# Optimization experiments

Measured on AMD Instinct MI355X. Metric: run time of the kernel, lower is better.

The kernel has to match this reference:

```python
import jax, jax.numpy as jnp
import numpy as np

B, S, D, H, DK, FF, NQ = 4, 1024, 512, 64, 8, 2048, 8


def _layernorm(x, w, b, eps=1e-5):
    m = x.mean(-1, keepdims=True)
    v = ((x - m) ** 2).mean(-1, keepdims=True)
    return (x - m) / jnp.sqrt(v + eps) * w + b


def setup_inputs() -> dict:
    key = jax.random.key(0)
    ks = jax.random.split(key, 24)
    std = 0.02
    inp = {
        "x": jax.random.normal(ks[0], (B, S, D), dtype=jnp.float32),
        "Wq": jax.random.normal(ks[1], (D, D)) * std,
        "bq": jnp.zeros((D,)),
        "Wk": jax.random.normal(ks[2], (D, D)) * std,
        "bk": jnp.zeros((D,)),
        "Wv": jax.random.normal(ks[3], (D, D)) * std,
        "bv": jnp.zeros((D,)),
        "theta_attn": jax.random.normal(ks[4], (DK,)) * 0.1,  # trainable RX angles
        "gate_attn": jnp.asarray(1.0, dtype=jnp.float32),
        "Wo": jax.random.normal(ks[5], (D, D)) * std,
        "bo": jnp.zeros((D,)),
        "ln1_w": jnp.ones((D,)),
        "ln1_b": jnp.zeros((D,)),
        "W1": jax.random.normal(ks[6], (FF, NQ)) * std,
        "b1": jnp.zeros((FF,)),
        "W2": jax.random.normal(ks[7], (D, FF)) * std,
        "b2": jnp.zeros((D,)),
        "phi_ffn": jax.random.normal(ks[8], (NQ,)) * 0.1,  # trainable RY angles
        "gate_ffn": jnp.asarray(1.0, dtype=jnp.float32),
        "ln2_w": jnp.ones((D,)),
        "ln2_b": jnp.zeros((D,)),
    }
    return inp


def _attention(x, Wq, bq, Wk, bk, Wv, bv, theta, gate, Wo, bo):
    q = x @ Wq.T + bq
    k = x @ Wk.T + bk
    v = x @ Wv.T + bv
    sep = lambda t: t.reshape(B, S, H, DK).transpose(0, 2, 1, 3)  # [B,H,S,DK]
    qh, kh, vh = sep(q), sep(k), sep(v)
    scores = jnp.einsum("bhsd,bhtd->bhst", qh, kh) / np.sqrt(DK)
    probs = jax.nn.softmax(scores, axis=-1)
    classical = jnp.einsum("bhst,bhtd->bhsd", probs, vh)
    classical = classical.transpose(0, 2, 1, 3).reshape(B, S, D)
    # Quantum head: RX(x_i) then RX(theta_i) -> RX(x_i+theta_i), CNOT ring, <Z_j>.
    # Analytic expectations: <Z_0> = prod_{k=1..DK-1} cos(a_k);
    #                        <Z_j> = prod_{k=0..j}    cos(a_k)   (j >= 1).
    cos_a = jnp.cos(qh + theta)  # [B,H,S,DK]
    cp = jnp.cumprod(cos_a, axis=-1)
    z0 = jnp.prod(cos_a[..., 1:], axis=-1, keepdims=True)
    quantum = jnp.concatenate([z0, cp[..., 1:]], axis=-1)  # [B,H,S,DK]
    quantum = quantum.transpose(0, 2, 1, 3).reshape(B, S, D)
    out = gate * quantum + (1.0 - gate) * classical
    return out @ Wo.T + bo


def _ffn(x, W1, b1, W2, b2, phi, gate):
    xs = x[..., :NQ]  # encoder uses first NQ features
    # Quantum: RX(x_i) then RY(phi_i), measure <Z_i> = cos(x_i)*cos(phi_i).
    qm = jnp.cos(xs) * jnp.cos(phi)
    quantum = jax.nn.relu(qm @ W1.T + b1) @ W2.T + b2
    classical = jax.nn.relu(xs @ W1.T + b1) @ W2.T + b2
    return gate * quantum + (1.0 - gate) * classical


def reference(x, Wq, bq, Wk, bk, Wv, bv, theta_attn, gate_attn, Wo, bo,
              ln1_w, ln1_b, W1, b1, W2, b2, phi_ffn, gate_ffn, ln2_w, ln2_b):
    attn_out = _attention(x, Wq, bq, Wk, bk, Wv, bv, theta_attn, gate_attn, Wo, bo)
    x1 = _layernorm(x + attn_out, ln1_w, ln1_b)
    ffn_out = _ffn(x1, W1, b1, W2, b2, phi_ffn, gate_ffn)
    return _layernorm(x1 + ffn_out, ln2_w, ln2_b)
```

## Files before the change

kernel.cpp:

```cpp
#include <hip/hip_runtime.h>
#include <hip/hip_bf16.h>


typedef short short8 __attribute__((ext_vector_type(8)));
typedef float floatx4 __attribute__((ext_vector_type(4)));

__device__ __forceinline__ unsigned short f2bf_bits(float f) {
  __hip_bfloat16 h = __float2bfloat16(f);
  return *reinterpret_cast<unsigned short*>(&h);
}
__device__ __forceinline__ float bfbits2f(unsigned short u) {
  union { unsigned int u; float f; } c;
  c.u = (unsigned int)u << 16;
  return c.f;
}

#define GLOBAL_LOAD_LDS16(g, l)                                               \
  __builtin_amdgcn_global_load_lds(                                           \
      (const __attribute__((address_space(1))) void*)(g),                     \
      (__attribute__((address_space(3))) void*)(l), 16, 0, 0)

#define WAIT_VMCNT0()   asm volatile("s_waitcnt vmcnt(0)" ::: "memory")
#define WAIT_VMCNT8()   asm volatile("s_waitcnt vmcnt(8)" ::: "memory")
#define WAIT_VMCNT10()  asm volatile("s_waitcnt vmcnt(10)" ::: "memory")
#define WAIT_VMCNT16()  asm volatile("s_waitcnt vmcnt(16)" ::: "memory")
#define WAIT_LGKM0()    asm volatile("s_waitcnt lgkmcnt(0)" ::: "memory")
#define BARRIER()       __builtin_amdgcn_s_barrier()
#define CFENCE()        asm volatile("" ::: "memory")

__device__ __forceinline__ void gemm_core_ks(
    const __hip_bfloat16* __restrict__ A,
    const __hip_bfloat16* __restrict__ W,
    int K, int kbeg, int ntiles, long m0, long n0, int lane,
    __hip_bfloat16* sh, floatx4 acc[4][4])
{
  const int srow = lane >> 3;
  const int gchunk = (lane & 7) ^ srow;
  const int frow = lane & 15;
  const int fk = lane >> 4;

  auto stage = [&](int kt, __hip_bfloat16* buf) {
#pragma unroll
    for (int ib = 0; ib < 8; ++ib) {
      const int row = ib * 8 + srow;
      GLOBAL_LOAD_LDS16(A + (m0 + row) * K + kt + gchunk * 8, buf + ib * 512);
      GLOBAL_LOAD_LDS16(W + (n0 + row) * K + kt + gchunk * 8, buf + 4096 + ib * 512);
    }
  };

  WAIT_LGKM0();
  stage(kbeg, sh);
  if (ntiles > 1) stage(kbeg + 64, sh + 8192);

  for (int t = 0; t < ntiles; ++t) {
    __hip_bfloat16* buf = sh + (t & 1) * 8192;
    if (t < ntiles - 1) { WAIT_VMCNT16(); }
    else               { WAIT_VMCNT0(); }

    short8 af[2][4], bf[2][4];
#pragma unroll
    for (int ks = 0; ks < 2; ++ks)
#pragma unroll
      for (int i = 0; i < 4; ++i) {
        const int ar = i * 16 + frow;
        af[ks][i] = *(const short8*)(buf + ar * 64 + (((ks * 4 + fk) ^ (ar & 7)) << 3));
        bf[ks][i] = *(const short8*)(buf + 4096 + ar * 64 + (((ks * 4 + fk) ^ (ar & 7)) << 3));
      }
    WAIT_LGKM0();
    if (t + 2 < ntiles) stage(kbeg + ((t + 2) << 6), buf);
#pragma unroll
    for (int ks = 0; ks < 2; ++ks)
#pragma unroll
      for (int i = 0; i < 4; ++i)
#pragma unroll
        for (int j = 0; j < 4; ++j)
          acc[i][j] = __builtin_amdgcn_mfma_f32_16x16x32_bf16(
              af[ks][i], bf[ks][j], acc[i][j], 0, 0, 0);
  }
}

__device__ __forceinline__ bool ks_reduce(
    floatx4 acc[4][4], __hip_bfloat16* sh, int wid, int lane)
{
  float* red = (float*)(sh + 16384);
  if (wid == 1) {
#pragma unroll
    for (int i = 0; i < 4; ++i)
#pragma unroll
      for (int j = 0; j < 4; ++j)
        *(floatx4*)(red + ((i * 4 + j) * 64 + lane) * 4) = acc[i][j];
    WAIT_LGKM0();
  }
  CFENCE(); BARRIER(); CFENCE();
  if (wid == 1) return false;
#pragma unroll
  for (int i = 0; i < 4; ++i)
#pragma unroll
    for (int j = 0; j < 4; ++j)
      acc[i][j] += *(const floatx4*)(red + ((i * 4 + j) * 64 + lane) * 4);
  return true;
}

__device__ __forceinline__ void store_f32(
    floatx4 acc[4][4], float* __restrict__ C, const float* __restrict__ bias,
    long m0, long n0, int lane)
{
  const int col_l = lane & 15;
  const int row_l = (lane >> 4) << 2;
#pragma unroll
  for (int j = 0; j < 4; ++j) {
    const long col = n0 + j * 16 + col_l;
    const float bv = bias[col];
#pragma unroll
    for (int i = 0; i < 4; ++i)
#pragma unroll
      for (int r = 0; r < 4; ++r)
        C[(m0 + i * 16 + row_l + r) * 512 + col] = acc[i][j][r] + bv;
  }
}

__device__ __forceinline__ void store_bf16(
    floatx4 acc[4][4], __hip_bfloat16* __restrict__ C,
    const float* __restrict__ bias, long m0, long n0, int lane)
{
  const int col_l = lane & 15;
  const int row_l = (lane >> 4) << 2;
#pragma unroll
  for (int j = 0; j < 4; ++j) {
    const long col = n0 + j * 16 + col_l;
    const float bv = bias[col];
#pragma unroll
    for (int i = 0; i < 4; ++i)
#pragma unroll
      for (int r = 0; r < 4; ++r)
        C[(m0 + i * 16 + row_l + r) * 512 + col] =
            __float2bfloat16(acc[i][j][r] + bv);
  }
}

__global__ __launch_bounds__(128) void gemm_qkv(
    const __hip_bfloat16* __restrict__ x_bf,
    const __hip_bfloat16* __restrict__ Wq,
    const __hip_bfloat16* __restrict__ Wk,
    const __hip_bfloat16* __restrict__ Wv,
    const float* __restrict__ bq, const float* __restrict__ bk,
    const float* __restrict__ bvv,
    __hip_bfloat16* __restrict__ mix,
    float* __restrict__ Qb, float* __restrict__ Kb, float* __restrict__ Vb,
    const float* __restrict__ theta, const float* __restrict__ gateA)
{
  const int z = blockIdx.z;
  const float g = *gateA;
  if (z > 0 && g == 1.0f) return;
  const __hip_bfloat16* W = (z == 0) ? Wq : (z == 1) ? Wk : Wv;
  const float* bias = (z == 0) ? bq : (z == 1) ? bk : bvv;
  float* Cf = (z == 0) ? Qb : (z == 1) ? Kb : Vb;

  __shared__ __align__(16) __hip_bfloat16 sh[32768];
  const int tid = threadIdx.x;
  const int wid = tid >> 6;
  const int lane = tid & 63;
  const long m0 = (long)blockIdx.x * 64;
  const long n0 = (long)blockIdx.y * 64;
  floatx4 acc[4][4];
#pragma unroll
  for (int i = 0; i < 4; ++i)
#pragma unroll
    for (int j = 0; j < 4; ++j) acc[i][j] = (floatx4){0.f, 0.f, 0.f, 0.f};

  gemm_core_ks(x_bf, W, 512, wid * 256, 4, m0, n0, lane, sh + wid * 16384, acc);
  if (!ks_reduce(acc, sh, wid, lane)) return;

  const int col_l = lane & 15;
  const int row_l = (lane >> 4) << 2;

  if (z > 0 || g != 1.0f) store_f32(acc, Cf, bias, m0, n0, lane);
  if (z == 0) {
    float* shf = (float*)sh;
    WAIT_LGKM0();
#pragma unroll
    for (int j = 0; j < 4; ++j) {
      const long col = n0 + j * 16 + col_l;
      const float bv = bias[col];
#pragma unroll
      for (int i = 0; i < 4; ++i)
#pragma unroll
        for (int r = 0; r < 4; ++r)
          shf[(i * 16 + row_l + r) * 64 + j * 16 + col_l] = acc[i][j][r] + bv;
    }
    WAIT_LGKM0();
    float th[8];
#pragma unroll
    for (int i = 0; i < 8; ++i) th[i] = theta[i];
#pragma unroll
    for (int t = 0; t < 8; ++t) {
      const int gidx = t * 64 + lane;
      const int row = gidx >> 3;
      const int hh = gidx & 7;
      const float* src = shf + row * 64 + hh * 8;
      float c[8];
#pragma unroll
      for (int i = 0; i < 8; ++i) c[i] = __cosf(src[i] + th[i]);
      float o[8];
      float p = c[1];
#pragma unroll
      for (int i = 2; i < 8; ++i) p *= c[i];
      o[0] = p;
      float cp = c[0];
#pragma unroll
      for (int i = 1; i < 8; ++i) { cp *= c[i]; o[i] = cp; }
      union { unsigned short u16[8]; uint4 v; } pk;
#pragma unroll
      for (int i = 0; i < 8; ++i) pk.u16[i] = f2bf_bits(o[i]);
      *(uint4*)(mix + (m0 + row) * 512 + n0 + hh * 8) = pk.v;
    }
  }
}

__global__ __launch_bounds__(512) void wo_lnffn(
    const __hip_bfloat16* __restrict__ A,
    const __hip_bfloat16* __restrict__ W,
    const float* __restrict__ bo,
    const float* __restrict__ x,
    const float* __restrict__ lw, const float* __restrict__ lb,
    float* __restrict__ x1, const float* __restrict__ phi,
    const float* __restrict__ W1,
    const float* __restrict__ b1,
    __hip_bfloat16* __restrict__ hq, __hip_bfloat16* __restrict__ hc,
    const float* __restrict__ gateF,
    __hip_bfloat16* __restrict__ mix_rw,
    const float* __restrict__ Qb, const float* __restrict__ Kb,
    const float* __restrict__ Vb, const float* __restrict__ gateA)
{
  __shared__ __align__(16) __hip_bfloat16 sh[68608];
  const int tid = threadIdx.x;
  const int wid = tid >> 6;
  const int lane = tid & 63;
  const long m0 = (long)blockIdx.x * 16;
  const long n0w = (long)wid * 64;

  const float g = *gateA;
  if (g != 1.0f) {
#pragma unroll 1
    for (int p = tid * 2; p < tid * 2 + 2; ++p) {
      const int r = p >> 6;
      const int h = p & 63;
      const long row = m0 + r;
      const int b = (int)(row >> 10);
      const long qoff = row * 512 + h * 8;
      float q[8];
#pragma unroll
      for (int i = 0; i < 8; ++i) q[i] = Qb[qoff + i] * 0.35355339059327373f;
      float m = -INFINITY, l = 0.0f, acc8[8];
#pragma unroll
      for (int i = 0; i < 8; ++i) acc8[i] = 0.0f;
      for (int t = 0; t < 1024; ++t) {
        const long koff = ((long)(b * 1024 + t)) * 512 + h * 8;
        const float* kr = Kb + koff;
        const float* vr = Vb + koff;
        float sc = 0.0f;
#pragma unroll
        for (int i = 0; i < 8; ++i) sc += q[i] * kr[i];
        float nm = fmaxf(m, sc);
        float corr = __expf(m - nm);
        float pp = __expf(sc - nm);
        l = l * corr + pp;
#pragma unroll
        for (int i = 0; i < 8; ++i) acc8[i] = acc8[i] * corr + pp * vr[i];
        m = nm;
      }
      const float inv = 1.0f / l;
      union { unsigned short u16[8]; uint4 v; } pk;
      pk.v = *(const uint4*)(mix_rw + qoff);
#pragma unroll
      for (int i = 0; i < 8; ++i) {
        float quant = bfbits2f(pk.u16[i]);
        pk.u16[i] = f2bf_bits(g * quant + (1.0f - g) * acc8[i] * inv);
      }
      *(uint4*)(mix_rw + qoff) = pk.v;
    }
    WAIT_VMCNT0();
    CFENCE(); BARRIER(); CFENCE();
  }

  const int srow = lane >> 3;
  const int gchunk = (lane & 7) ^ srow;
  const int frow = lane & 15;
  const int fk = lane >> 4;

  __hip_bfloat16* shA = sh;
  __hip_bfloat16* shW = sh + 3072 + wid * 8192;

  auto stageA = [&](int kt, int slot) {
    __hip_bfloat16* buf = shA + slot * 1024;
#pragma unroll
    for (int i = 0; i < 2; ++i) {
      const int row = i * 8 + srow;
      GLOBAL_LOAD_LDS16(A + (m0 + row) * 512 + kt + gchunk * 8, buf + i * 512);
    }
  };
  auto stageW = [&](int kt, int slot) {
    __hip_bfloat16* buf = shW + slot * 4096;
#pragma unroll
    for (int i = 0; i < 8; ++i) {
      const int row = i * 8 + srow;
      GLOBAL_LOAD_LDS16(W + (n0w + row) * 512 + kt + gchunk * 8, buf + i * 512);
    }
  };

  floatx4 acc[4];
#pragma unroll
  for (int j = 0; j < 4; ++j) acc[j] = (floatx4){0.f, 0.f, 0.f, 0.f};

  if (wid == 0) stageA(0, 0);
  stageW(0, 0);
  if (wid == 0) stageA(64, 1);
  stageW(64, 1);

  for (int t = 0; t < 8; ++t) {
    const int wslot = t & 1;
    const int aslot = t % 3;
    if (t < 7) { if (wid == 0) WAIT_VMCNT10(); else WAIT_VMCNT8(); }
    else       { WAIT_VMCNT0(); }
    BARRIER();

    short8 af[2], bf[2][4];
#pragma unroll
    for (int ks = 0; ks < 2; ++ks) {
      af[ks] = *(const short8*)(shA + aslot * 1024 + frow * 64 +
                                (((ks * 4 + fk) ^ (frow & 7)) << 3));
#pragma unroll
      for (int j = 0; j < 4; ++j) {
        const int wr = j * 16 + frow;
        bf[ks][j] = *(const short8*)(shW + wslot * 4096 + wr * 64 +
                                     (((ks * 4 + fk) ^ (wr & 7)) << 3));
      }
    }
    WAIT_LGKM0();
    if (t < 6) {
      if (wid == 0) stageA((t + 2) << 6, (t + 2) % 3);
      stageW((t + 2) << 6, wslot);
    }
#pragma unroll
    for (int ks = 0; ks < 2; ++ks)
#pragma unroll
      for (int j = 0; j < 4; ++j)
        acc[j] = __builtin_amdgcn_mfma_f32_16x16x32_bf16(
            af[ks], bf[ks][j], acc[j], 0, 0, 0);
  }

  BARRIER();

  float* attnL = (float*)sh;
  float* qmL = attnL + 16 * 516;
  float* xsL = qmL + 128;
  {
    const int col_l = lane & 15;
    const int row_l = (lane >> 4) << 2;
#pragma unroll
    for (int j = 0; j < 4; ++j) {
      const int c = (int)n0w + j * 16 + col_l;
      const float bv = bo[c];
#pragma unroll
      for (int r = 0; r < 4; ++r)
        attnL[(row_l + r) * 516 + c] = acc[j][r] + bv;
    }
  }
  WAIT_LGKM0();
  BARRIER();

  const int rr = tid >> 5;
  const int cl = tid & 31;
  const long rowg = m0 + rr;
  float sv[16];
  float sum = 0.f, ssq = 0.f;
#pragma unroll
  for (int i = 0; i < 16; ++i) {
    const int c = cl + i * 32;
    const float v = x[rowg * 512 + c] + attnL[rr * 516 + c];
    sv[i] = v; sum += v; ssq += v * v;
  }
#pragma unroll
  for (int off = 16; off > 0; off >>= 1) {
    sum += __shfl_xor(sum, off, 32);
    ssq += __shfl_xor(ssq, off, 32);
  }
  const float mean = sum * (1.0f / 512.0f);
  const float var = ssq * (1.0f / 512.0f) - mean * mean;
  const float rstd = rsqrtf(fmaxf(var, 0.0f) + 1e-5f);
#pragma unroll
  for (int i = 0; i < 16; ++i) {
    const int c = cl + i * 32;
    const float o = (sv[i] - mean) * rstd * lw[c] + lb[c];
    x1[rowg * 512 + c] = o;
    if (i == 0 && cl < 8) {
      qmL[rr * 8 + cl] = __cosf(o) * __cosf(phi[cl]);
      xsL[rr * 8 + cl] = o;
    }
  }
  WAIT_LGKM0();
  BARRIER();

  const int n4 = tid << 2;
  float w1r[4][8];
#pragma unroll
  for (int jr = 0; jr < 4; ++jr) {
    float4 wa = *(const float4*)(W1 + (long)(n4 + jr) * 8);
    float4 wb = *(const float4*)(W1 + (long)(n4 + jr) * 8 + 4);
    w1r[jr][0] = wa.x; w1r[jr][1] = wa.y; w1r[jr][2] = wa.z; w1r[jr][3] = wa.w;
    w1r[jr][4] = wb.x; w1r[jr][5] = wb.y; w1r[jr][6] = wb.z; w1r[jr][7] = wb.w;
  }
  float4 bb = *(const float4*)(b1 + n4);
  const float b1a[4] = {bb.x, bb.y, bb.z, bb.w};
  const float gv = *gateF;
#pragma unroll 2
  for (int r = 0; r < 16; ++r) {
    float qm8[8];
#pragma unroll
    for (int k = 0; k < 8; ++k) qm8[k] = qmL[r * 8 + k];
    union { unsigned short u16[4]; ushort4 v; } pk;
#pragma unroll
    for (int jr = 0; jr < 4; ++jr) {
      float a = b1a[jr];
#pragma unroll
      for (int k = 0; k < 8; ++k) a += qm8[k] * w1r[jr][k];
      pk.u16[jr] = f2bf_bits(fmaxf(a, 0.0f));
    }
    *(ushort4*)(hq + (m0 + r) * 2048 + n4) = pk.v;
    if (gv != 1.0f) {
      float xs8[8];
#pragma unroll
      for (int k = 0; k < 8; ++k) xs8[k] = xsL[r * 8 + k];
#pragma unroll
      for (int jr = 0; jr < 4; ++jr) {
        float a = b1a[jr];
#pragma unroll
        for (int k = 0; k < 8; ++k) a += xs8[k] * w1r[jr][k];
        pk.u16[jr] = f2bf_bits(fmaxf(a, 0.0f));
      }
      *(ushort4*)(hc + (m0 + r) * 2048 + n4) = pk.v;
    }
  }
}

__global__ __launch_bounds__(128) void gemm_ffnout(
    const __hip_bfloat16* __restrict__ hq,
    const __hip_bfloat16* __restrict__ hc,
    const __hip_bfloat16* __restrict__ W2, const float* __restrict__ b2,
    __hip_bfloat16* __restrict__ Fb, __hip_bfloat16* __restrict__ Fc,
    const float* __restrict__ gateF)
{
  const int z = blockIdx.z;
  if (z == 1 && *gateF == 1.0f) return;
  const __hip_bfloat16* A = z ? hc : hq;
  __hip_bfloat16* C = z ? Fc : Fb;
  __shared__ __align__(16) __hip_bfloat16 sh[32768];
  const int tid = threadIdx.x;
  const int wid = tid >> 6;
  const int lane = tid & 63;
  const long m0 = (long)blockIdx.x * 64;
  const long n0 = (long)blockIdx.y * 64;
  floatx4 acc[4][4];
#pragma unroll
  for (int i = 0; i < 4; ++i)
#pragma unroll
    for (int j = 0; j < 4; ++j) acc[i][j] = (floatx4){0.f, 0.f, 0.f, 0.f};
  gemm_core_ks(A, W2, 2048, wid * 1024, 16, m0, n0, lane, sh + wid * 16384, acc);
  if (!ks_reduce(acc, sh, wid, lane)) return;
  store_bf16(acc, C, b2, m0, n0, lane);
}

__device__ __forceinline__ void cvt_one(const float* s, __hip_bfloat16* d, int n,
                                        long tid, long stride) {
  const int n4 = n >> 2;
  for (long i = tid; i < n4; i += stride) {
    float4 v = ((const float4*)s)[i];
    ushort4 u;
    u.x = f2bf_bits(v.x); u.y = f2bf_bits(v.y);
    u.z = f2bf_bits(v.z); u.w = f2bf_bits(v.w);
    ((ushort4*)d)[i] = u;
  }
}

__global__ __launch_bounds__(256) void prep_inputs(
    const float* x, __hip_bfloat16* x_bf,
    const float* Wq, __hip_bfloat16* Wq_bf,
    const float* Wo, __hip_bfloat16* Wo_bf,
    const float* W2, __hip_bfloat16* W2_bf,
    const float* Wk, __hip_bfloat16* Wk_bf,
    const float* Wv, __hip_bfloat16* Wv_bf,
    const float* gateA)
{
  const long stride = (long)gridDim.x * blockDim.x;
  const long tid = (long)blockIdx.x * blockDim.x + threadIdx.x;
  cvt_one(x, x_bf, 4096 * 512, tid, stride);
  cvt_one(Wq, Wq_bf, 512 * 512, tid, stride);
  cvt_one(Wo, Wo_bf, 512 * 512, tid, stride);
  cvt_one(W2, W2_bf, 512 * 2048, tid, stride);
  if (*gateA != 1.0f) {
    cvt_one(Wk, Wk_bf, 512 * 512, tid, stride);
    cvt_one(Wv, Wv_bf, 512 * 512, tid, stride);
  }
}

__global__ __launch_bounds__(256) void add_ln3(
    const float* __restrict__ x1, const __hip_bfloat16* __restrict__ Fb,
    const __hip_bfloat16* __restrict__ Fc, const float* __restrict__ gateF,
    const float* __restrict__ lw, const float* __restrict__ lb,
    float* __restrict__ out)
{
  const int tid = threadIdx.x;
  const int wv = tid >> 6, lane = tid & 63;
  const int row = blockIdx.x * 4 + wv;
  const long base = (long)row * 512;
  const int c0 = lane * 8;
  float4 a0 = *(const float4*)(x1 + base + c0);
  float4 a1 = *(const float4*)(x1 + base + c0 + 4);
  union { unsigned short u16[8]; uint4 v; } fb;
  fb.v = *(const uint4*)(Fb + base + c0);
  const float xa[8] = {a0.x, a0.y, a0.z, a0.w, a1.x, a1.y, a1.z, a1.w};
  float s[8];
  const float gv = *gateF;
  if (gv != 1.0f) {
    union { unsigned short u16[8]; uint4 v; } fc;
    fc.v = *(const uint4*)(Fc + base + c0);
    const float om = 1.0f - gv;
#pragma unroll
    for (int i = 0; i < 8; ++i)
      s[i] = xa[i] + gv * bfbits2f(fb.u16[i]) + om * bfbits2f(fc.u16[i]);
  } else {
#pragma unroll
    for (int i = 0; i < 8; ++i) s[i] = xa[i] + bfbits2f(fb.u16[i]);
  }
  float sum = 0.f, ssq = 0.f;
#pragma unroll
  for (int i = 0; i < 8; ++i) { sum += s[i]; ssq += s[i] * s[i]; }
#pragma unroll
  for (int off = 32; off > 0; off >>= 1) {
    sum += __shfl_xor(sum, off);
    ssq += __shfl_xor(ssq, off);
  }
  const float mean = sum * (1.0f / 512.0f);
  const float var = ssq * (1.0f / 512.0f) - mean * mean;
  const float rstd = rsqrtf(fmaxf(var, 0.0f) + 1e-5f);
  float4 w0 = *(const float4*)(lw + c0);
  float4 w1 = *(const float4*)(lw + c0 + 4);
  float4 g0 = *(const float4*)(lb + c0);
  float4 g1 = *(const float4*)(lb + c0 + 4);
  const float wf[8] = {w0.x, w0.y, w0.z, w0.w, w1.x, w1.y, w1.z, w1.w};
  const float gf8[8] = {g0.x, g0.y, g0.z, g0.w, g1.x, g1.y, g1.z, g1.w};
  float o[8];
#pragma unroll
  for (int i = 0; i < 8; ++i) o[i] = (s[i] - mean) * rstd * wf[i] + gf8[i];
  *(float4*)(out + base + c0) = (float4){o[0], o[1], o[2], o[3]};
  *(float4*)(out + base + c0 + 4) = (float4){o[4], o[5], o[6], o[7]};
}

extern "C" void kernel_launch(void* const* d_in, const int* in_sizes, int n_in,
                              void* d_out, int out_size, void* d_ws, size_t ws_size,
                              hipStream_t stream) {
  const float* x     = (const float*)d_in[0];
  const float* Wq    = (const float*)d_in[1];
  const float* bq    = (const float*)d_in[2];
  const float* Wk    = (const float*)d_in[3];
  const float* bk    = (const float*)d_in[4];
  const float* Wv    = (const float*)d_in[5];
  const float* bv    = (const float*)d_in[6];
  const float* theta = (const float*)d_in[7];
  const float* gateA = (const float*)d_in[8];
  const float* Wo    = (const float*)d_in[9];
  const float* bo    = (const float*)d_in[10];
  const float* ln1w  = (const float*)d_in[11];
  const float* ln1b  = (const float*)d_in[12];
  const float* W1    = (const float*)d_in[13];
  const float* b1    = (const float*)d_in[14];
  const float* W2    = (const float*)d_in[15];
  const float* b2    = (const float*)d_in[16];
  const float* phi   = (const float*)d_in[17];
  const float* gateF = (const float*)d_in[18];
  const float* ln2w  = (const float*)d_in[19];
  const float* ln2b  = (const float*)d_in[20];
  float* out = (float*)d_out;

  const size_t MB = 1024 * 1024;
  char* wsb = (char*)d_ws;
  __hip_bfloat16* x_bf    = (__hip_bfloat16*)(wsb + 0 * MB);
  __hip_bfloat16* Wq_bf   = (__hip_bfloat16*)(wsb + 4 * MB);
  __hip_bfloat16* Wo_bf   = (__hip_bfloat16*)(wsb + 4 * MB + 512 * 1024);
  __hip_bfloat16* W2_bf   = (__hip_bfloat16*)(wsb + 5 * MB);
  __hip_bfloat16* mix_bf  = (__hip_bfloat16*)(wsb + 8 * MB);
  float*          x1      = (float*)(wsb + 16 * MB);
  __hip_bfloat16* hq_bf   = (__hip_bfloat16*)(wsb + 24 * MB);
  __hip_bfloat16* Fb_bf   = (__hip_bfloat16*)(wsb + 40 * MB);
  float*          Qb      = (float*)(wsb + 52 * MB);
  __hip_bfloat16* Wk_bf   = (__hip_bfloat16*)(wsb + 60 * MB);
  __hip_bfloat16* Wv_bf   = (__hip_bfloat16*)(wsb + 60 * MB + 512 * 1024);
  float*          Kb2     = (float*)(wsb + 61 * MB);
  float*          Vb2     = (float*)(wsb + 69 * MB);
  __hip_bfloat16* hc_bf   = (__hip_bfloat16*)(wsb + 77 * MB);
  __hip_bfloat16* Fc_bf   = (__hip_bfloat16*)(wsb + 93 * MB);

  prep_inputs<<<1024, 256, 0, stream>>>(
      x, x_bf, Wq, Wq_bf, Wo, Wo_bf, W2, W2_bf, Wk, Wk_bf, Wv, Wv_bf, gateA);
  gemm_qkv<<<dim3(64, 8, 3), 128, 0, stream>>>(
      x_bf, Wq_bf, Wk_bf, Wv_bf, bq, bk, bv,
      mix_bf, Qb, Kb2, Vb2, theta, gateA);
  wo_lnffn<<<256, 512, 0, stream>>>(
      mix_bf, Wo_bf, bo, x, ln1w, ln1b, x1, phi, W1, b1, hq_bf, hc_bf, gateF,
      mix_bf, Qb, Kb2, Vb2, gateA);
  gemm_ffnout<<<dim3(64, 8, 2), 128, 0, stream>>>(
      hq_bf, hc_bf, W2_bf, b2, Fb_bf, Fc_bf, gateF);
  add_ln3<<<1024, 256, 0, stream>>>(x1, Fb_bf, Fc_bf, gateF, ln2w, ln2b, out);
}
```

Baseline: 143.4 us.

## Fuse final add+LayerNorm into FFN-out GEMM via last-block atomic counter

```diff
diff --git a/kernel.cpp b/kernel.cpp
--- a/kernel.cpp
+++ b/kernel.cpp
@@ -448,13 +448,18 @@
     const __hip_bfloat16* __restrict__ hc,
     const __hip_bfloat16* __restrict__ W2, const float* __restrict__ b2,
     __hip_bfloat16* __restrict__ Fb, __hip_bfloat16* __restrict__ Fc,
-    const float* __restrict__ gateF)
+    const float* __restrict__ gateF,
+    const float* __restrict__ x1, const float* __restrict__ lw,
+    const float* __restrict__ lb, float* __restrict__ out,
+    int* __restrict__ cnt)
 {
   const int z = blockIdx.z;
-  if (z == 1 && *gateF == 1.0f) return;
+  const float gv = *gateF;
+  if (z == 1 && gv == 1.0f) return;
   const __hip_bfloat16* A = z ? hc : hq;
   __hip_bfloat16* C = z ? Fc : Fb;
   __shared__ __align__(16) __hip_bfloat16 sh[32768];
+  __shared__ int lastFlag;
   const int tid = threadIdx.x;
   const int wid = tid >> 6;
   const int lane = tid & 63;
@@ -466,8 +471,63 @@
 #pragma unroll
     for (int j = 0; j < 4; ++j) acc[i][j] = (floatx4){0.f, 0.f, 0.f, 0.f};
   gemm_core_ks(A, W2, 2048, wid * 1024, 16, m0, n0, lane, sh + wid * 16384, acc);
-  if (!ks_reduce(acc, sh, wid, lane)) return;
-  store_bf16(acc, C, b2, m0, n0, lane);
+  const bool w0 = ks_reduce(acc, sh, wid, lane);
+  if (w0) store_bf16(acc, C, b2, m0, n0, lane);
+
+  __threadfence();
+  if (tid == 0) {
+    const int target = (gv != 1.0f) ? 16 : 8;
+    lastFlag = (atomicAdd(&cnt[blockIdx.x], 1) == target - 1) ? 1 : 0;
+  }
+  __syncthreads();
+  if (!lastFlag) return;
+  __threadfence();
+
+#pragma unroll 1
+  for (int it = 0; it < 32; ++it) {
+    const long row = m0 + it * 2 + wid;
+    const long base = row * 512;
+    const int c0 = lane * 8;
+    float4 a0 = *(const float4*)(x1 + base + c0);
+    float4 a1 = *(const float4*)(x1 + base + c0 + 4);
+    union { unsigned short u16[8]; uint4 v; } fb;
+    fb.v = *(const uint4*)(Fb + base + c0);
+    const float xa[8] = {a0.x, a0.y, a0.z, a0.w, a1.x, a1.y, a1.z, a1.w};
+    float s[8];
+    if (gv != 1.0f) {
+      union { unsigned short u16[8]; uint4 v; } fc;
+      fc.v = *(const uint4*)(Fc + base + c0);
+      const float om = 1.0f - gv;
+#pragma unroll
+      for (int i = 0; i < 8; ++i)
+        s[i] = xa[i] + gv * bfbits2f(fb.u16[i]) + om * bfbits2f(fc.u16[i]);
+    } else {
+#pragma unroll
+      for (int i = 0; i < 8; ++i) s[i] = xa[i] + bfbits2f(fb.u16[i]);
+    }
+    float sum = 0.f, ssq = 0.f;
+#pragma unroll
+    for (int i = 0; i < 8; ++i) { sum += s[i]; ssq += s[i] * s[i]; }
+#pragma unroll
+    for (int off = 32; off > 0; off >>= 1) {
+      sum += __shfl_xor(sum, off);
+      ssq += __shfl_xor(ssq, off);
+    }
+    const float mean = sum * (1.0f / 512.0f);
+    const float var = ssq * (1.0f / 512.0f) - mean * mean;
+    const float rstd = rsqrtf(fmaxf(var, 0.0f) + 1e-5f);
+    float4 w0v = *(const float4*)(lw + c0);
+    float4 w1v = *(const float4*)(lw + c0 + 4);
+    float4 g0 = *(const float4*)(lb + c0);
+    float4 g1 = *(const float4*)(lb + c0 + 4);
+    const float wf[8] = {w0v.x, w0v.y, w0v.z, w0v.w, w1v.x, w1v.y, w1v.z, w1v.w};
+    const float gf8[8] = {g0.x, g0.y, g0.z, g0.w, g1.x, g1.y, g1.z, g1.w};
+    float o[8];
+#pragma unroll
+    for (int i = 0; i < 8; ++i) o[i] = (s[i] - mean) * rstd * wf[i] + gf8[i];
+    *(float4*)(out + base + c0) = (float4){o[0], o[1], o[2], o[3]};
+    *(float4*)(out + base + c0 + 4) = (float4){o[4], o[5], o[6], o[7]};
+  }
 }
 
 __device__ __forceinline__ void cvt_one(const float* s, __hip_bfloat16* d, int n,
@@ -489,10 +549,11 @@
     const float* W2, __hip_bfloat16* W2_bf,
     const float* Wk, __hip_bfloat16* Wk_bf,
     const float* Wv, __hip_bfloat16* Wv_bf,
-    const float* gateA)
+    const float* gateA, int* cnt)
 {
   const long stride = (long)gridDim.x * blockDim.x;
   const long tid = (long)blockIdx.x * blockDim.x + threadIdx.x;
+  if (blockIdx.x == 0 && threadIdx.x < 64) cnt[threadIdx.x] = 0;
   cvt_one(x, x_bf, 4096 * 512, tid, stride);
   cvt_one(Wq, Wq_bf, 512 * 512, tid, stride);
   cvt_one(Wo, Wo_bf, 512 * 512, tid, stride);
@@ -501,59 +562,6 @@
     cvt_one(Wk, Wk_bf, 512 * 512, tid, stride);
     cvt_one(Wv, Wv_bf, 512 * 512, tid, stride);
   }
-}
-
-__global__ __launch_bounds__(256) void add_ln3(
-    const float* __restrict__ x1, const __hip_bfloat16* __restrict__ Fb,
-    const __hip_bfloat16* __restrict__ Fc, const float* __restrict__ gateF,
-    const float* __restrict__ lw, const float* __restrict__ lb,
-    float* __restrict__ out)
-{
-  const int tid = threadIdx.x;
-  const int wv = tid >> 6, lane = tid & 63;
-  const int row = blockIdx.x * 4 + wv;
-  const long base = (long)row * 512;
-  const int c0 = lane * 8;
-  float4 a0 = *(const float4*)(x1 + base + c0);
-  float4 a1 = *(const float4*)(x1 + base + c0 + 4);
-  union { unsigned short u16[8]; uint4 v; } fb;
-  fb.v = *(const uint4*)(Fb + base + c0);
-  const float xa[8] = {a0.x, a0.y, a0.z, a0.w, a1.x, a1.y, a1.z, a1.w};
-  float s[8];
-  const float gv = *gateF;
-  if (gv != 1.0f) {
-    union { unsigned short u16[8]; uint4 v; } fc;
-    fc.v = *(const uint4*)(Fc + base + c0);
-    const float om = 1.0f - gv;
-#pragma unroll
-    for (int i = 0; i < 8; ++i)
-      s[i] = xa[i] + gv * bfbits2f(fb.u16[i]) + om * bfbits2f(fc.u16[i]);
-  } else {
-#pragma unroll
-    for (int i = 0; i < 8; ++i) s[i] = xa[i] + bfbits2f(fb.u16[i]);
-  }
-  float sum = 0.f, ssq = 0.f;
-#pragma unroll
-  for (int i = 0; i < 8; ++i) { sum += s[i]; ssq += s[i] * s[i]; }
-#pragma unroll
-  for (int off = 32; off > 0; off >>= 1) {
-    sum += __shfl_xor(sum, off);
-    ssq += __shfl_xor(ssq, off);
-  }
-  const float mean = sum * (1.0f / 512.0f);
-  const float var = ssq * (1.0f / 512.0f) - mean * mean;
-  const float rstd = rsqrtf(fmaxf(var, 0.0f) + 1e-5f);
-  float4 w0 = *(const float4*)(lw + c0);
-  float4 w1 = *(const float4*)(lw + c0 + 4);
-  float4 g0 = *(const float4*)(lb + c0);
-  float4 g1 = *(const float4*)(lb + c0 + 4);
-  const float wf[8] = {w0.x, w0.y, w0.z, w0.w, w1.x, w1.y, w1.z, w1.w};
-  const float gf8[8] = {g0.x, g0.y, g0.z, g0.w, g1.x, g1.y, g1.z, g1.w};
-  float o[8];
-#pragma unroll
-  for (int i = 0; i < 8; ++i) o[i] = (s[i] - mean) * rstd * wf[i] + gf8[i];
-  *(float4*)(out + base + c0) = (float4){o[0], o[1], o[2], o[3]};
-  *(float4*)(out + base + c0 + 4) = (float4){o[4], o[5], o[6], o[7]};
 }
 
 extern "C" void kernel_launch(void* const* d_in, const int* in_sizes, int n_in,
@@ -592,6 +600,7 @@
   float*          x1      = (float*)(wsb + 16 * MB);
   __hip_bfloat16* hq_bf   = (__hip_bfloat16*)(wsb + 24 * MB);
   __hip_bfloat16* Fb_bf   = (__hip_bfloat16*)(wsb + 40 * MB);
+  int*            cnt     = (int*)(wsb + 48 * MB);
   float*          Qb      = (float*)(wsb + 52 * MB);
   __hip_bfloat16* Wk_bf   = (__hip_bfloat16*)(wsb + 60 * MB);
   __hip_bfloat16* Wv_bf   = (__hip_bfloat16*)(wsb + 60 * MB + 512 * 1024);
@@ -601,7 +610,8 @@
   __hip_bfloat16* Fc_bf   = (__hip_bfloat16*)(wsb + 93 * MB);
 
   prep_inputs<<<1024, 256, 0, stream>>>(
-      x, x_bf, Wq, Wq_bf, Wo, Wo_bf, W2, W2_bf, Wk, Wk_bf, Wv, Wv_bf, gateA);
+      x, x_bf, Wq, Wq_bf, Wo, Wo_bf, W2, W2_bf, Wk, Wk_bf, Wv, Wv_bf,
+      gateA, cnt);
   gemm_qkv<<<dim3(64, 8, 3), 128, 0, stream>>>(
       x_bf, Wq_bf, Wk_bf, Wv_bf, bq, bk, bv,
       mix_bf, Qb, Kb2, Vb2, theta, gateA);
@@ -609,6 +619,6 @@
       mix_bf, Wo_bf, bo, x, ln1w, ln1b, x1, phi, W1, b1, hq_bf, hc_bf, gateF,
       mix_bf, Qb, Kb2, Vb2, gateA);
   gemm_ffnout<<<dim3(64, 8, 2), 128, 0, stream>>>(
-      hq_bf, hc_bf, W2_bf, b2, Fb_bf, Fc_bf, gateF);
-  add_ln3<<<1024, 256, 0, stream>>>(x1, Fb_bf, Fc_bf, gateF, ln2w, ln2b, out);
-}
+      hq_bf, hc_bf, W2_bf, b2, Fb_bf, Fc_bf, gateF,
+      x1, ln2w, ln2b, out, cnt);
+}
```

Measured after the change: 189.8 us. 1.32x slower.
